# Optimization experiments

Measured on AMD Instinct MI355X. Metric: run time of the kernel, lower is better.

The kernel has to match this reference:

```python
import jax, jax.numpy as jnp
import numpy as np

N_NODES = 20000
N_EDGES = 320000
D_IN = 256
DIMS = [512, 256, 128]
NEG_SLOPE = 0.2


def gatv2(x, src, dst, Wl, Wr, att, b, n):
    # GATv2Conv (heads=1, no self loops, no edge_attr)
    xl = x @ Wl                      # [N, D] source transform (lin_l)
    xr = x @ Wr                      # [N, D] target transform (lin_r)
    e = jax.nn.leaky_relu(xl[src] + xr[dst], NEG_SLOPE) @ att  # [E]
    # segment softmax over destination nodes
    m = jax.ops.segment_max(e, dst, num_segments=n)
    ex = jnp.exp(e - m[dst])
    s = jax.ops.segment_sum(ex, dst, num_segments=n)
    alpha = ex / (s[dst] + 1e-16)
    out = jax.ops.segment_sum(alpha[:, None] * xl[src], dst, num_segments=n)
    return out + b


def setup_inputs() -> dict:
    key = jax.random.key(0)
    ks = jax.random.split(key, 32)
    x = jax.random.normal(ks[0], (N_NODES, D_IN), dtype=jnp.float32)
    edge_index = jax.random.randint(ks[1], (2, N_EDGES), 0, N_NODES, dtype=jnp.int32)
    inp = {"x": x, "edge_index": edge_index}
    d_in = D_IN
    ki = 2
    for li, d_out in enumerate(DIMS, start=1):
        sc = 1.0 / np.sqrt(d_in)
        inp[f"Wl{li}"] = jax.random.normal(ks[ki + 0], (d_in, d_out), dtype=jnp.float32) * sc
        inp[f"Wr{li}"] = jax.random.normal(ks[ki + 1], (d_in, d_out), dtype=jnp.float32) * sc
        inp[f"att{li}"] = jax.random.normal(ks[ki + 2], (d_out,), dtype=jnp.float32) * (1.0 / np.sqrt(d_out))
        inp[f"bc{li}"] = jnp.zeros((d_out,), dtype=jnp.float32)
        inp[f"Ws{li}"] = jax.random.normal(ks[ki + 3], (d_in, d_out), dtype=jnp.float32) * sc
        inp[f"bs{li}"] = jnp.zeros((d_out,), dtype=jnp.float32)
        ki += 4
        d_in = d_out
    return inp


def reference(x, edge_index,
              Wl1, Wr1, att1, bc1, Ws1, bs1,
              Wl2, Wr2, att2, bc2, Ws2, bs2,
              Wl3, Wr3, att3, bc3, Ws3, bs3):
    src, dst = edge_index[0], edge_index[1]
    n = x.shape[0]
    h = gatv2(x, src, dst, Wl1, Wr1, att1, bc1, n) + (x @ Ws1 + bs1)
    h = jax.nn.relu(h)
    h = gatv2(h, src, dst, Wl2, Wr2, att2, bc2, n) + (h @ Ws2 + bs2)
    h = jax.nn.relu(h)
    h = gatv2(h, src, dst, Wl3, Wr3, att3, bc3, n) + (h @ Ws3 + bs3)
    return h
```

## Files before the change

### kernel.cpp

```cpp
#include <hip/hip_runtime.h>
#include <hip/hip_bf16.h>
#include <math.h>

#define N_NODES 20000
#define N_EDGES 320000

typedef _Float16 f16x8 __attribute__((ext_vector_type(8)));
typedef _Float16 h2 __attribute__((ext_vector_type(2)));
typedef float f32x4 __attribute__((ext_vector_type(4)));

__device__ __forceinline__ unsigned short f2h_bits(float f) {
    _Float16 h = (_Float16)f;
    return __builtin_bit_cast(unsigned short, h);
}

typedef const unsigned int __attribute__((address_space(1)))* gas_ptr;
typedef unsigned int __attribute__((address_space(3)))* las_ptr;
__device__ __forceinline__ void gld16(const unsigned short* g, unsigned short* l) {
    __builtin_amdgcn_global_load_lds((gas_ptr)(const void*)g, (las_ptr)(void*)l, 16, 0, 0);
}

__global__ void zero_int_kernel(int* __restrict__ p, int n) {
    int i = blockIdx.x * blockDim.x + threadIdx.x;
    if (i < n) p[i] = 0;
}

__global__ void count_deg_kernel(const int* __restrict__ dst, int* __restrict__ deg, int E) {
    int i = blockIdx.x * blockDim.x + threadIdx.x;
    if (i < E) atomicAdd(&deg[dst[i]], 1);
}

#define SCAN_T 1024
#define SCAN_C 20
__global__ __launch_bounds__(1024) void scan_kernel(const int* __restrict__ deg,
                                                    int* __restrict__ offs,
                                                    int* __restrict__ cursor, int n) {
    __shared__ int sd[SCAN_T];
    int t = threadIdx.x;
    int base = t * SCAN_C;
    int vex[SCAN_C];
    int run = 0;
#pragma unroll
    for (int k = 0; k < SCAN_C; ++k) {
        int i = base + k;
        int d = (i < n) ? deg[i] : 0;
        vex[k] = run;
        run += d;
    }
    sd[t] = run;
    __syncthreads();
    for (int off = 1; off < SCAN_T; off <<= 1) {
        int x = (t >= off) ? sd[t - off] : 0;
        __syncthreads();
        sd[t] += x;
        __syncthreads();
    }
    int excl = sd[t] - run;
#pragma unroll
    for (int k = 0; k < SCAN_C; ++k) {
        int i = base + k;
        if (i < n) { int e = excl + vex[k]; offs[i] = e; cursor[i] = e; }
    }
    if (t == SCAN_T - 1) offs[n] = sd[t];
}

__global__ void scatter_kernel(const int* __restrict__ src, const int* __restrict__ dst,
                               int* __restrict__ cursor, int* __restrict__ csr_src, int E) {
    int i = blockIdx.x * blockDim.x + threadIdx.x;
    if (i < E) {
        int pos = atomicAdd(&cursor[dst[i]], 1);
        csr_src[pos] = src[i];
    }
}

__global__ void convert_f16_kernel(const float* __restrict__ in,
                                   unsigned short* __restrict__ out, int n) {
    int i = blockIdx.x * blockDim.x + threadIdx.x;
    int base = i * 4;
    if (base + 3 < n) {
        float4 v = *(const float4*)(in + base);
        uint2 pk;
        pk.x = (unsigned int)f2h_bits(v.x) | ((unsigned int)f2h_bits(v.y) << 16);
        pk.y = (unsigned int)f2h_bits(v.z) | ((unsigned int)f2h_bits(v.w) << 16);
        *(uint2*)(out + base) = pk;
    } else {
        for (int k = base; k < n; ++k) out[k] = f2h_bits(in[k]);
    }
}

struct TransJobs {
    const float* W[9];
    unsigned short* Wt[9];
    int K[9];
    int D[9];
    int beg[10];
};
__global__ void transpose_all_kernel(TransJobs jb) {
    int i = blockIdx.x * blockDim.x + threadIdx.x;
    if (i >= jb.beg[9]) return;
    int job = 0;
    while (i >= jb.beg[job + 1]) ++job;
    int local = i - jb.beg[job];
    int D = jb.D[job], K = jb.K[job];
    int d = local / K, k = local - d * K;
    jb.Wt[job][local] = f2h_bits(jb.W[job][(size_t)k * D + d]);
}

template <int SEED_F32>
__global__ __launch_bounds__(256) void gemm3_kernel(
        const unsigned short* __restrict__ A,
        const unsigned short* __restrict__ Bt,
        unsigned short* __restrict__ xlh,
        unsigned short* __restrict__ xrh,
        unsigned short* __restrict__ seedh,
        float* __restrict__ seedf,
        const float* __restrict__ b1,
        const float* __restrict__ b2,
        int M, int K, int D) {
    __shared__ __align__(16) unsigned short Asl[128 * 32];
    __shared__ __align__(16) unsigned short Bsl[128 * 32];

    int tid = threadIdx.x;
    int wave = tid >> 6, lane = tid & 63;
    int q = lane >> 4, t = lane & 15;
    int wm = (wave & 1) * 64, wn = (wave >> 1) * 64;
    int bm = blockIdx.y * 128;
    int bn_all = blockIdx.x * 128;
    int seg = bn_all / D;
    int bn = bn_all - seg * D;

    f32x4 acc[4][4];
#pragma unroll
    for (int i = 0; i < 4; ++i)
#pragma unroll
        for (int j = 0; j < 4; ++j) acc[i][j] = (f32x4){0.f, 0.f, 0.f, 0.f};

    for (int k0 = 0; k0 < K; k0 += 32) {
#pragma unroll
        for (int rnd = 0; rnd < 2; ++rnd) {
            int c = rnd * 256 + tid;
            int row = c >> 2, part = c & 3;
            int gr = bm + row; if (gr >= M) gr = M - 1;
            gld16(A + (size_t)gr * K + k0 + part * 8,
                  Asl + (rnd * 256 + wave * 64) * 8);
        }
#pragma unroll
        for (int rnd = 0; rnd < 2; ++rnd) {
            int c = rnd * 256 + tid;
            int row = c >> 2, part = c & 3;
            gld16(Bt + (size_t)(bn_all + row) * K + k0 + part * 8,
                  Bsl + (rnd * 256 + wave * 64) * 8);
        }
        __syncthreads();

        f16x8 an[4], am[4];
#pragma unroll
        for (int jn = 0; jn < 4; ++jn)
            an[jn] = *(const f16x8*)(Bsl + (wn + jn * 16 + t) * 32 + q * 8);
#pragma unroll
        for (int im = 0; im < 4; ++im)
            am[im] = *(const f16x8*)(Asl + (wm + im * 16 + t) * 32 + q * 8);
#pragma unroll
        for (int jn = 0; jn < 4; ++jn)
#pragma unroll
            for (int im = 0; im < 4; ++im)
                acc[jn][im] = __builtin_amdgcn_mfma_f32_16x16x32_f16(an[jn], am[im], acc[jn][im], 0, 0, 0);
        __syncthreads();
    }

#pragma unroll
    for (int jn = 0; jn < 4; ++jn) {
        int n0 = bn + wn + jn * 16 + q * 4;
        float bx = 0.f, by = 0.f, bz = 0.f, bw = 0.f;
        if (seg == 2) {
            float4 bb1 = *(const float4*)(b1 + n0);
            float4 bb2 = *(const float4*)(b2 + n0);
            bx = bb1.x + bb2.x; by = bb1.y + bb2.y;
            bz = bb1.z + bb2.z; bw = bb1.w + bb2.w;
        }
#pragma unroll
        for (int im = 0; im < 4; ++im) {
            int m = bm + wm + im * 16 + t;
            if (m < M) {
                float v0 = acc[jn][im][0] + bx;
                float v1 = acc[jn][im][1] + by;
                float v2 = acc[jn][im][2] + bz;
                float v3 = acc[jn][im][3] + bw;
                size_t idx = (size_t)m * D + n0;
                if (seg == 2 && SEED_F32) {
                    *(float4*)(seedf + idx) = make_float4(v0, v1, v2, v3);
                } else {
                    uint2 pk;
                    pk.x = (unsigned int)f2h_bits(v0) | ((unsigned int)f2h_bits(v1) << 16);
                    pk.y = (unsigned int)f2h_bits(v2) | ((unsigned int)f2h_bits(v3) << 16);
                    unsigned short* dstp = (seg == 0) ? xlh : (seg == 1) ? xrh : seedh;
                    *(uint2*)(dstp + idx) = pk;
                }
            }
        }
    }
}

template <int D, int SEED_H, int WRITE_H, int RELU>
__global__ __launch_bounds__(256) void fused_agg_kernel(
        const unsigned short* __restrict__ xl,
        const unsigned short* __restrict__ xr,
        const float* __restrict__ att,
        const int* __restrict__ offs,
        const int* __restrict__ csr_src,
        const unsigned short* __restrict__ seedh,
        const float* __restrict__ seedf,
        float* __restrict__ outf,
        unsigned short* __restrict__ outh) {
    constexpr int VPL = D / 64;
    constexpr int HP = VPL / 2;
    typedef _Float16 hvec __attribute__((ext_vector_type(VPL)));

    int wave = threadIdx.x >> 6, lane = threadIdx.x & 63;
    int n = blockIdx.x * 4 + wave;
    if (n >= N_NODES) return;
    int beg = offs[n], end = offs[n + 1];

    h2 xr_h[HP], att_h[HP];
    hvec xrv = *(const hvec*)(xr + (size_t)n * D + lane * VPL);
#pragma unroll
    for (int pp = 0; pp < HP; ++pp) {
        xr_h[pp] = (h2){xrv[2 * pp], xrv[2 * pp + 1]};
        att_h[pp] = (h2){(_Float16)att[lane * VPL + 2 * pp],
                         (_Float16)att[lane * VPL + 2 * pp + 1]};
    }

    float acc[VPL];
#pragma unroll
    for (int v = 0; v < VPL; ++v) acc[v] = 0.f;
    float m = -INFINITY, s = 0.f;

    const _Float16 c02 = (_Float16)0.2f;
    int lb0 = lane & 1;
    int lb1 = lane & 2;

    int j = beg;
    for (; j + 3 < end; j += 4) {
        int s0 = csr_src[j], s1 = csr_src[j + 1], s2 = csr_src[j + 2], s3 = csr_src[j + 3];
        hvec x0 = *(const hvec*)(xl + (size_t)s0 * D + lane * VPL);
        hvec x1 = *(const hvec*)(xl + (size_t)s1 * D + lane * VPL);
        hvec x2 = *(const hvec*)(xl + (size_t)s2 * D + lane * VPL);
        hvec x3 = *(const hvec*)(xl + (size_t)s3 * D + lane * VPL);
        float p0 = 0.f, p1 = 0.f, p2 = 0.f, p3 = 0.f;
#pragma unroll
        for (int pp = 0; pp < HP; ++pp) {
            h2 a0 = (h2){x0[2 * pp], x0[2 * pp + 1]};
            h2 a1 = (h2){x1[2 * pp], x1[2 * pp + 1]};
            h2 a2 = (h2){x2[2 * pp], x2[2 * pp + 1]};
            h2 a3 = (h2){x3[2 * pp], x3[2 * pp + 1]};
            h2 z0 = a0 + xr_h[pp];
            h2 z1 = a1 + xr_h[pp];
            h2 z2 = a2 + xr_h[pp];
            h2 z3 = a3 + xr_h[pp];
            h2 l0 = __builtin_elementwise_max(z0, z0 * c02);
            h2 l1 = __builtin_elementwise_max(z1, z1 * c02);
            h2 l2 = __builtin_elementwise_max(z2, z2 * c02);
            h2 l3 = __builtin_elementwise_max(z3, z3 * c02);
#if __has_builtin(__builtin_amdgcn_fdot2)
            p0 = __builtin_amdgcn_fdot2(l0, att_h[pp], p0, false);
            p1 = __builtin_amdgcn_fdot2(l1, att_h[pp], p1, false);
            p2 = __builtin_amdgcn_fdot2(l2, att_h[pp], p2, false);
            p3 = __builtin_amdgcn_fdot2(l3, att_h[pp], p3, false);
#else
            p0 += (float)l0.x * (float)att_h[pp].x + (float)l0.y * (float)att_h[pp].y;
            p1 += (float)l1.x * (float)att_h[pp].x + (float)l1.y * (float)att_h[pp].y;
            p2 += (float)l2.x * (float)att_h[pp].x + (float)l2.y * (float)att_h[pp].y;
            p3 += (float)l3.x * (float)att_h[pp].x + (float)l3.y * (float)att_h[pp].y;
#endif
        }
        float k0 = lb0 ? p1 : p0, sn0 = lb0 ? p0 : p1;
        float k1 = lb0 ? p3 : p2, sn1 = lb0 ? p2 : p3;
        k0 += __shfl_xor(sn0, 1, 64);
        k1 += __shfl_xor(sn1, 1, 64);
        float k = lb1 ? k1 : k0, sn = lb1 ? k0 : k1;
        k += __shfl_xor(sn, 2, 64);
        k += __shfl_xor(k, 4, 64);
        k += __shfl_xor(k, 8, 64);
        k += __shfl_xor(k, 16, 64);
        k += __shfl_xor(k, 32, 64);
        float q0 = __shfl(k, 0, 64);
        float q1 = __shfl(k, 1, 64);
        float q2 = __shfl(k, 2, 64);
        float q3 = __shfl(k, 3, 64);

        float mn = fmaxf(m, fmaxf(fmaxf(q0, q1), fmaxf(q2, q3)));
        float sc = __expf(m - mn);
        float e0 = __expf(q0 - mn);
        float e1 = __expf(q1 - mn);
        float e2 = __expf(q2 - mn);
        float e3 = __expf(q3 - mn);
        s = s * sc + e0 + e1 + e2 + e3;
#pragma unroll
        for (int v = 0; v < VPL; ++v)
            acc[v] = acc[v] * sc + e0 * (float)x0[v] + e1 * (float)x1[v]
                                 + e2 * (float)x2[v] + e3 * (float)x3[v];
        m = mn;
    }
    for (; j < end; ++j) {
        int s0 = csr_src[j];
        hvec x0 = *(const hvec*)(xl + (size_t)s0 * D + lane * VPL);
        float p0 = 0.f;
#pragma unroll
        for (int pp = 0; pp < HP; ++pp) {
            h2 a0 = (h2){x0[2 * pp], x0[2 * pp + 1]};
            h2 z0 = a0 + xr_h[pp];
            h2 l0 = __builtin_elementwise_max(z0, z0 * c02);
#if __has_builtin(__builtin_amdgcn_fdot2)
            p0 = __builtin_amdgcn_fdot2(l0, att_h[pp], p0, false);
#else
            p0 += (float)l0.x * (float)att_h[pp].x + (float)l0.y * (float)att_h[pp].y;
#endif
        }
#pragma unroll
        for (int o = 32; o > 0; o >>= 1) p0 += __shfl_xor(p0, o, 64);
        float mn = fmaxf(m, p0);
        float sc = __expf(m - mn);
        float e0 = __expf(p0 - mn);
        s = s * sc + e0;
#pragma unroll
        for (int v = 0; v < VPL; ++v) acc[v] = acc[v] * sc + e0 * (float)x0[v];
        m = mn;
    }

    float sinv = 1.0f / (s + 1e-16f);
    size_t base = (size_t)n * D + lane * VPL;
    float sd[VPL];
    if (SEED_H) {
        hvec sv = *(const hvec*)(seedh + base);
#pragma unroll
        for (int v = 0; v < VPL; ++v) sd[v] = (float)sv[v];
    } else {
#pragma unroll
        for (int v = 0; v < VPL; ++v) sd[v] = seedf[base + v];
    }
#pragma unroll
    for (int v = 0; v < VPL; ++v) {
        float val = sd[v] + acc[v] * sinv;
        if (RELU) val = fmaxf(val, 0.f);
        if (WRITE_H) outh[base + v] = f2h_bits(val);
        else         outf[base + v] = val;
    }
}

static void run_layer(const unsigned short* hact, int K, int D,
                      const unsigned short* Wcat,
                      const float* att, const float* bc, const float* bs,
                      unsigned short* xlh, unsigned short* xrh,
                      unsigned short* seedh, float* seedf,
                      const int* offs, const int* csr_src,
                      float* outf, unsigned short* outh, int final_layer,
                      hipStream_t stream) {
    dim3 ggrid(3 * D / 128, (N_NODES + 127) / 128);
    if (final_layer)
        hipLaunchKernelGGL((gemm3_kernel<1>), ggrid, dim3(256), 0, stream, hact, Wcat,
                           xlh, xrh, (unsigned short*)nullptr, seedf, bs, bc, N_NODES, K, D);
    else
        hipLaunchKernelGGL((gemm3_kernel<0>), ggrid, dim3(256), 0, stream, hact, Wcat,
                           xlh, xrh, seedh, (float*)nullptr, bs, bc, N_NODES, K, D);

    dim3 agrid((N_NODES + 3) / 4);
    if (D == 512) {
        hipLaunchKernelGGL((fused_agg_kernel<512, 1, 1, 1>), agrid, dim3(256), 0, stream,
                           xlh, xrh, att, offs, csr_src, seedh, (const float*)nullptr,
                           (float*)nullptr, outh);
    } else if (D == 256) {
        hipLaunchKernelGGL((fused_agg_kernel<256, 1, 1, 1>), agrid, dim3(256), 0, stream,
                           xlh, xrh, att, offs, csr_src, seedh, (const float*)nullptr,
                           (float*)nullptr, outh);
    } else {
        hipLaunchKernelGGL((fused_agg_kernel<128, 0, 0, 0>), agrid, dim3(256), 0, stream,
                           xlh, xrh, att, offs, csr_src, (const unsigned short*)nullptr, seedf,
                           outf, (unsigned short*)nullptr);
    }
}

extern "C" void kernel_launch(void* const* d_in, const int* in_sizes, int n_in,
                              void* d_out, int out_size, void* d_ws, size_t ws_size,
                              hipStream_t stream) {
    const float* x = (const float*)d_in[0];
    const int* ei = (const int*)d_in[1];
    const int* src = ei;
    const int* dst = ei + N_EDGES;

    const float* Wl1 = (const float*)d_in[2];
    const float* Wr1 = (const float*)d_in[3];
    const float* att1 = (const float*)d_in[4];
    const float* bc1 = (const float*)d_in[5];
    const float* Ws1 = (const float*)d_in[6];
    const float* bs1 = (const float*)d_in[7];
    const float* Wl2 = (const float*)d_in[8];
    const float* Wr2 = (const float*)d_in[9];
    const float* att2 = (const float*)d_in[10];
    const float* bc2 = (const float*)d_in[11];
    const float* Ws2 = (const float*)d_in[12];
    const float* bs2 = (const float*)d_in[13];
    const float* Wl3 = (const float*)d_in[14];
    const float* Wr3 = (const float*)d_in[15];
    const float* att3 = (const float*)d_in[16];
    const float* bc3 = (const float*)d_in[17];
    const float* Ws3 = (const float*)d_in[18];
    const float* bs3 = (const float*)d_in[19];

    const size_t NF = (size_t)N_NODES * 512;
    const size_t NH = (size_t)N_NODES * 256;
    unsigned short* xlh   = (unsigned short*)d_ws;
    unsigned short* xrh   = xlh + NF;
    unsigned short* seedh = xrh + NF;
    unsigned short* xhf   = seedh + NF;
    unsigned short* h1h   = xhf + NH;
    unsigned short* h2h   = h1h + NF;
    unsigned short* Wcat1 = h2h + NH;
    unsigned short* Wcat2 = Wcat1 + 3 * 512 * 256;
    unsigned short* Wcat3 = Wcat2 + 3 * 256 * 512;
    int* deg     = (int*)(Wcat3 + 3 * 128 * 256);
    int* offs    = deg + N_NODES;
    int* cursor  = offs + N_NODES + 1;
    int* csr_src = cursor + N_NODES;
    size_t needed = (size_t)((char*)(csr_src + N_EDGES) - (char*)d_ws);
    if (ws_size < needed) return;

    hipLaunchKernelGGL(zero_int_kernel, dim3((N_NODES + 255) / 256), dim3(256), 0, stream,
                       deg, N_NODES);
    hipLaunchKernelGGL(count_deg_kernel, dim3((N_EDGES + 255) / 256), dim3(256), 0, stream,
                       dst, deg, N_EDGES);
    hipLaunchKernelGGL(scan_kernel, dim3(1), dim3(SCAN_T), 0, stream, deg, offs, cursor, N_NODES);
    hipLaunchKernelGGL(scatter_kernel, dim3((N_EDGES + 255) / 256), dim3(256), 0, stream,
                       src, dst, cursor, csr_src, N_EDGES);

    {
        TransJobs jb;
        const float* Ws_[9]  = {Wl1, Wr1, Ws1, Wl2, Wr2, Ws2, Wl3, Wr3, Ws3};
        unsigned short* Wt_[9] = {Wcat1, Wcat1 + 512 * 256, Wcat1 + 2 * 512 * 256,
                                  Wcat2, Wcat2 + 256 * 512, Wcat2 + 2 * 256 * 512,
                                  Wcat3, Wcat3 + 128 * 256, Wcat3 + 2 * 128 * 256};
        int K_[9] = {256, 256, 256, 512, 512, 512, 256, 256, 256};
        int D_[9] = {512, 512, 512, 256, 256, 256, 128, 128, 128};
        int o = 0;
        for (int i = 0; i < 9; ++i) {
            jb.W[i] = Ws_[i]; jb.Wt[i] = Wt_[i]; jb.K[i] = K_[i]; jb.D[i] = D_[i];
            jb.beg[i] = o; o += K_[i] * D_[i];
        }
        jb.beg[9] = o;
        hipLaunchKernelGGL(transpose_all_kernel, dim3((o + 255) / 256), dim3(256), 0, stream, jb);
    }

    {
        int nconv = N_NODES * 256;
        hipLaunchKernelGGL(convert_f16_kernel, dim3((nconv / 4 + 255) / 256), dim3(256), 0, stream,
                           x, xhf, nconv);
    }

    run_layer(xhf, 256, 512, Wcat1, att1, bc1, bs1,
              xlh, xrh, seedh, (float*)nullptr, offs, csr_src,
              (float*)nullptr, h1h, 0, stream);
    run_layer(h1h, 512, 256, Wcat2, att2, bc2, bs2,
              xlh, xrh, seedh, (float*)nullptr, offs, csr_src,
              (float*)nullptr, h2h, 0, stream);
    run_layer(h2h, 256, 128, Wcat3, att3, bc3, bs3,
              xlh, xrh, (unsigned short*)nullptr, (float*)d_out, offs, csr_src,
              (float*)d_out, (unsigned short*)nullptr, 1, stream);
}
```

Baseline: 375.2 us.

## Remap GEMM blocks XCD-aware and prefetch CSR indices in aggregation loop

The GEMM grid becomes 1D, with block IDs remapped so that all column tiles for a given row tile land on the same XCD (block id mod 8). This should improve L2 reuse of A rows across the XCDs' separate L2 caches. The aggregation kernel also software-prefetches the next group of four csr_src indices one iteration ahead, hiding index-load latency before the dependent gathers. The costs are a few padded blocks that exit early and slightly more registers in the aggregation loop.

Result: no change. 370.3 us (-1.3%).

```diff
diff --git a/kernel.cpp b/kernel.cpp
--- a/kernel.cpp
+++ b/kernel.cpp
@@ -120,12 +120,20 @@
     __shared__ __align__(16) unsigned short Asl[128 * 32];
     __shared__ __align__(16) unsigned short Bsl[128 * 32];
 
+    int NC = (3 * D) >> 7;
+    int MT = (M + 127) >> 7;
+    int g = blockIdx.x;
+    int xcd = g & 7, slot = g >> 3;
+    int m_local = slot / NC, c = slot - m_local * NC;
+    int mt = m_local * 8 + xcd;
+    if (mt >= MT) return;
+
     int tid = threadIdx.x;
     int wave = tid >> 6, lane = tid & 63;
     int q = lane >> 4, t = lane & 15;
     int wm = (wave & 1) * 64, wn = (wave >> 1) * 64;
-    int bm = blockIdx.y * 128;
-    int bn_all = blockIdx.x * 128;
+    int bm = mt << 7;
+    int bn_all = c << 7;
     int seg = bn_all / D;
     int bn = bn_all - seg * D;
 
@@ -138,16 +146,16 @@
     for (int k0 = 0; k0 < K; k0 += 32) {
 #pragma unroll
         for (int rnd = 0; rnd < 2; ++rnd) {
-            int c = rnd * 256 + tid;
-            int row = c >> 2, part = c & 3;
+            int ch = rnd * 256 + tid;
+            int row = ch >> 2, part = ch & 3;
             int gr = bm + row; if (gr >= M) gr = M - 1;
             gld16(A + (size_t)gr * K + k0 + part * 8,
                   Asl + (rnd * 256 + wave * 64) * 8);
         }
 #pragma unroll
         for (int rnd = 0; rnd < 2; ++rnd) {
-            int c = rnd * 256 + tid;
-            int row = c >> 2, part = c & 3;
+            int ch = rnd * 256 + tid;
+            int row = ch >> 2, part = ch & 3;
             gld16(Bt + (size_t)(bn_all + row) * K + k0 + part * 8,
                   Bsl + (rnd * 256 + wave * 64) * 8);
         }
@@ -239,9 +247,20 @@
     int lb0 = lane & 1;
     int lb1 = lane & 2;
 
+    int nfull = (end - beg) >> 2;
     int j = beg;
-    for (; j + 3 < end; j += 4) {
-        int s0 = csr_src[j], s1 = csr_src[j + 1], s2 = csr_src[j + 2], s3 = csr_src[j + 3];
+    int i0 = 0, i1 = 0, i2 = 0, i3 = 0;
+    if (nfull > 0) {
+        i0 = csr_src[beg]; i1 = csr_src[beg + 1];
+        i2 = csr_src[beg + 2]; i3 = csr_src[beg + 3];
+    }
+    for (int b = 0; b < nfull; ++b) {
+        int s0 = i0, s1 = i1, s2 = i2, s3 = i3;
+        int jn4 = j + 4;
+        if (b + 1 < nfull) {
+            i0 = csr_src[jn4]; i1 = csr_src[jn4 + 1];
+            i2 = csr_src[jn4 + 2]; i3 = csr_src[jn4 + 3];
+        }
         hvec x0 = *(const hvec*)(xl + (size_t)s0 * D + lane * VPL);
         hvec x1 = *(const hvec*)(xl + (size_t)s1 * D + lane * VPL);
         hvec x2 = *(const hvec*)(xl + (size_t)s2 * D + lane * VPL);
@@ -300,6 +319,7 @@
             acc[v] = acc[v] * sc + e0 * (float)x0[v] + e1 * (float)x1[v]
                                  + e2 * (float)x2[v] + e3 * (float)x3[v];
         m = mn;
+        j = jn4;
     }
     for (; j < end; ++j) {
         int s0 = csr_src[j];
@@ -355,12 +375,14 @@
                       const int* offs, const int* csr_src,
                       float* outf, unsigned short* outh, int final_layer,
                       hipStream_t stream) {
-    dim3 ggrid(3 * D / 128, (N_NODES + 127) / 128);
+    int NC = 3 * D / 128;
+    int MT = (N_NODES + 127) / 128;
+    int nblk = 8 * ((MT + 7) / 8) * NC;
     if (final_layer)
-        hipLaunchKernelGGL((gemm3_kernel<1>), ggrid, dim3(256), 0, stream, hact, Wcat,
+        hipLaunchKernelGGL((gemm3_kernel<1>), dim3(nblk), dim3(256), 0, stream, hact, Wcat,
                            xlh, xrh, (unsigned short*)nullptr, seedf, bs, bc, N_NODES, K, D);
     else
-        hipLaunchKernelGGL((gemm3_kernel<0>), ggrid, dim3(256), 0, stream, hact, Wcat,
+        hipLaunchKernelGGL((gemm3_kernel<0>), dim3(nblk), dim3(256), 0, stream, hact, Wcat,
                            xlh, xrh, seedh, (float*)nullptr, bs, bc, N_NODES, K, D);
 
     dim3 agrid((N_NODES + 3) / 4);
```
